# Optimization experiments

Measured on AMD Instinct MI355X. Metric: run time of the kernel, lower is better.

## Reference

```python
import jax, jax.numpy as jnp
import numpy as np

EMBED_DIM = 512
BLOCK = 511
N_HEAD = 8
N_GLOBAL = 4
N_LOCAL = 2
N_MIX = 2
RECEP = 4
T = 2 * BLOCK + 2  # [task, clip, BLOCK upper, BLOCK lower]
HD = EMBED_DIM // N_HEAD
NEG = -1e9


def _build_masks():
    bs = BLOCK
    temporal = np.concatenate([np.zeros(2), np.arange(bs) * 2 + 1, np.arange(bs) * 2 + 2])
    seq = temporal[None, :] <= temporal[:, None]  # causal over interleaved temporal order
    tq = np.concatenate([np.arange(bs) * 2 + 1 - 2 * RECEP + 1] * 2)
    tk = np.concatenate([np.arange(bs) * 2 + 1] * 2)
    de = tk[None, :] < tq[:, None]  # keys too far in the past for the sliding window
    local = seq.copy()
    local[2:, 2:] = local[2:, 2:] & ~de
    return jnp.asarray(local), jnp.asarray(seq)


LOCAL_MASK, GLOBAL_MASK = _build_masks()  # (T, T) bool, True = visible


def _linear_params(key, fan_in, fan_out):
    k1, k2 = jax.random.split(key)
    s = 1.0 / np.sqrt(fan_in)
    W = jax.random.uniform(k1, (fan_out, fan_in), minval=-s, maxval=s, dtype=jnp.float32)
    b = jax.random.uniform(k2, (fan_out,), minval=-s, maxval=s, dtype=jnp.float32)
    return W, b


def setup_inputs() -> dict:
    key = jax.random.key(0)
    ks = jax.random.split(key, 10)
    B = 4
    x = jax.random.normal(ks[0], (B, T, EMBED_DIM), dtype=jnp.float32)
    cond_mask = jnp.ones((B, T), dtype=jnp.float32)
    Wq, bq = _linear_params(ks[1], EMBED_DIM, EMBED_DIM)
    Wk, bk = _linear_params(ks[2], EMBED_DIM, EMBED_DIM)
    Wv, bv = _linear_params(ks[3], EMBED_DIM, EMBED_DIM)
    Wqml, bqml = _linear_params(ks[4], EMBED_DIM, HD * N_MIX)
    Wkml, bkml = _linear_params(ks[5], EMBED_DIM, HD * N_MIX)
    Wp, bp = _linear_params(ks[6], EMBED_DIM, EMBED_DIM)
    mix_w = jax.random.normal(ks[7], (N_MIX, 2), dtype=jnp.float32) * 0.5  # Conv2d(2*nm, nm, groups=nm, 1x1)
    bias_clip = jnp.full((1, N_HEAD, 1), 0.5, dtype=jnp.float32)
    bias_clip_ml = jnp.full((1, N_MIX, 1), 0.5, dtype=jnp.float32)
    return dict(x=x, cond_mask=cond_mask, Wq=Wq, bq=bq, Wk=Wk, bk=bk, Wv=Wv, bv=bv,
                Wqml=Wqml, bqml=bqml, Wkml=Wkml, bkml=bkml, mix_w=mix_w, Wp=Wp, bp=bp,
                bias_clip=bias_clip, bias_clip_ml=bias_clip_ml)


def reference(x, cond_mask, Wq, bq, Wk, bk, Wv, bv, Wqml, bqml, Wkml, bkml, mix_w, Wp, bp, bias_clip, bias_clip_ml):
    B, Tx, C = x.shape

    def heads(W, b, nh):
        return (x @ W.T + b).reshape(B, Tx, nh, HD).transpose(0, 2, 1, 3)  # (B, nh, T, hd)

    q = heads(Wq, bq, N_HEAD)
    k = heads(Wk, bk, N_HEAD)
    v = heads(Wv, bv, N_HEAD)
    qml = heads(Wqml, bqml, N_MIX)
    kml = heads(Wkml, bkml, N_MIX)

    scale = 1.0 / np.sqrt(HD)
    # main attention: heads [0:N_LOCAL] local-masked, rest global (causal) masked
    att = jnp.einsum('bhqd,bhkd->bhqk', q, k) * scale
    att = att.at[:, :, :, 1].add(bias_clip)  # learned bias on the CLIP-token key column
    head_mask = jnp.concatenate([
        jnp.broadcast_to(LOCAL_MASK, (N_LOCAL, Tx, Tx)),
        jnp.broadcast_to(GLOBAL_MASK, (N_MIX + N_GLOBAL, Tx, Tx))], axis=0)
    att = jax.nn.softmax(jnp.where(head_mask[None], att, NEG), axis=-1)

    # extra local-masked score maps for the mix heads
    aml = jnp.einsum('bhqd,bhkd->bhqk', qml, kml) * scale
    aml = aml.at[:, :, :, 1].add(bias_clip_ml)
    aml = jax.nn.softmax(jnp.where(LOCAL_MASK[None, None], aml, NEG), axis=-1)

    # grouped 1x1 conv: per mix head, blend (global, local) attention maps
    mix_in = jnp.stack([att[:, N_LOCAL:N_LOCAL + N_MIX], aml], axis=2)  # (B, nm, 2, T, T)
    mix_out = jnp.einsum('ho,bhoqk->bhqk', mix_w, mix_in)

    att_f = jnp.concatenate([att[:, :N_LOCAL], mix_out, att[:, N_LOCAL + N_MIX:]], axis=1)
    y = jnp.einsum('bhqk,bhkd->bhqd', att_f, v)
    y = y.transpose(0, 2, 1, 3).reshape(B, Tx, C)
    return y @ Wp.T + bp
```

## Files before the change

kernel.cpp:

```cpp
#include <hip/hip_runtime.h>

typedef unsigned short u16;
typedef __attribute__((ext_vector_type(8))) __bf16 bf16x8;
typedef __attribute__((ext_vector_type(4))) float f32x4;
typedef __attribute__((ext_vector_type(8))) short short8;
typedef __attribute__((ext_vector_type(4))) u16 us4;

#define T_SEQ 1024
#define PW 1280

__device__ __forceinline__ u16 f2bf(float f) {
  unsigned u = __float_as_uint(f);
  u += 0x7fff + ((u >> 16) & 1);
  return (u16)(u >> 16);
}
__device__ __forceinline__ float bf2f(u16 v) {
  return __uint_as_float((unsigned)v << 16);
}

__constant__ u16 GLOB_M[16] = {0x0101,0x0303,0x0707,0x0F0F,0x1F1F,0x3F3F,0x7F7F,0xFFFF,
                               0xFFFF,0x0307,0x070F,0x0F1F,0x1F3F,0x3F7F,0x7FFF,0xFFFF};
__constant__ u16 LOC_M[16]  = {0x0101,0x0303,0x0607,0x0C0D,0x1819,0x3031,0x6061,0xC0C1,
                               0x8183,0x0307,0x060F,0x0C1D,0x1839,0x3071,0x60E1,0xC1C1};

__device__ __forceinline__ void gll16(const u16* gp, u16* lp) {
  __builtin_amdgcn_global_load_lds((const __attribute__((address_space(1))) unsigned*)gp,
                                   (__attribute__((address_space(3))) unsigned*)lp, 16, 0, 0);
}

template<int NISS>
__device__ __forceinline__ void stage_sw(u16* lds, const u16* __restrict__ g,
                                         int ld, int tid) {
  const int w = tid >> 6;
#pragma unroll
  for (int i = 0; i < NISS; ++i) {
    int row = i * 32 + (tid >> 3);
    int cswz = ((tid & 7) << 4) ^ ((row & 7) << 4);
    gll16(g + (size_t)row * ld + (cswz >> 1), lds + i * 2048 + w * 512);
  }
}

__device__ __forceinline__ bf16x8 rd_sw(const u16* lds, int row, int colbyte) {
  return *(const bf16x8*)&lds[row * 64 + ((colbyte ^ ((row & 7) << 4)) >> 1)];
}

__global__ void prep_all(const float4* __restrict__ x, u16* __restrict__ xb,
                         const float* __restrict__ Wq, const float* __restrict__ Wk,
                         const float* __restrict__ Wv, const float* __restrict__ Wqml,
                         const float* __restrict__ Wkml, const float* __restrict__ Wp,
                         const float* __restrict__ bq, const float* __restrict__ bk,
                         const float* __restrict__ bv, const float* __restrict__ bqml,
                         const float* __restrict__ bkml,
                         u16* __restrict__ Wcat, u16* __restrict__ Wpx, float* __restrict__ bcat) {
  if (blockIdx.x < 2048) {
    int i = blockIdx.x * 256 + threadIdx.x;
    float4 v = x[i];
    us4 o = { f2bf(v.x), f2bf(v.y), f2bf(v.z), f2bf(v.w) };
    *(us4*)&xb[i * 4] = o;
    return;
  }
  int idx = (blockIdx.x - 2048) * 256 + threadIdx.x;
  const int NW = 1792 * 512;
  if (idx < NW) {
    int row = idx >> 9;
    float v;
    if (row < 512)       v = Wq[idx];
    else if (row < 1024) v = Wk[idx - 512 * 512];
    else if (row < 1536) v = Wv[idx - 1024 * 512];
    else if (row < 1664) v = Wqml[idx - 1536 * 512];
    else                 v = Wkml[idx - 1664 * 512];
    Wcat[idx] = f2bf(v);
    return;
  }
  int i2 = idx - NW;
  if (i2 < 512 * 640) {
    int n = i2 / 640, k2 = i2 - n * 640;
    float v = (k2 < 512) ? Wp[n * 512 + k2] : Wp[n * 512 + k2 - 384];
    Wpx[i2] = f2bf(v);
    return;
  }
  int i3 = i2 - 512 * 640;
  if (i3 < 1792) {
    float v;
    if (i3 < 512)       v = bq[i3];
    else if (i3 < 1024) v = bk[i3 - 512];
    else if (i3 < 1536) v = bv[i3 - 1024];
    else if (i3 < 1664) v = bqml[i3 - 1536];
    else                v = bkml[i3 - 1664];
    bcat[i3] = v;
  }
}

__global__ __launch_bounds__(256) void gemm_qkv(
    const u16* __restrict__ A, const u16* __restrict__ Bw,
    const float* __restrict__ bias, u16* __restrict__ Pout, u16* __restrict__ Vtb) {
  __shared__ u16 As[2][8192];
  __shared__ u16 Bs[2][8192];
  const int tid = threadIdx.x;
  const int lane = tid & 63, w = tid >> 6;
  const int g = lane >> 4, c = lane & 15;
  const int n0 = blockIdx.x * 128, m0 = blockIdx.y * 128;
  const int wm = (w >> 1) * 64, wn = (w & 1) * 64;

  f32x4 acc[4][4] = {};
  stage_sw<4>(As[0], A + (size_t)m0 * 512, 512, tid);
  stage_sw<4>(Bs[0], Bw + (size_t)n0 * 512, 512, tid);
  __syncthreads();
  for (int ks = 0; ks < 8; ++ks) {
    int cur = ks & 1;
    if (ks + 1 < 8) {
      stage_sw<4>(As[cur ^ 1], A + (size_t)m0 * 512 + (ks + 1) * 64, 512, tid);
      stage_sw<4>(Bs[cur ^ 1], Bw + (size_t)n0 * 512 + (ks + 1) * 64, 512, tid);
    }
#pragma unroll
    for (int h = 0; h < 2; ++h) {
      bf16x8 av[4], bv[4];
#pragma unroll
      for (int f = 0; f < 4; ++f) {
        av[f] = rd_sw(As[cur], wm + f * 16 + c, h * 64 + g * 16);
        bv[f] = rd_sw(Bs[cur], wn + f * 16 + c, h * 64 + g * 16);
      }
#pragma unroll
      for (int fm = 0; fm < 4; ++fm)
#pragma unroll
        for (int fn = 0; fn < 4; ++fn)
          acc[fm][fn] = __builtin_amdgcn_mfma_f32_16x16x32_bf16(av[fm], bv[fn], acc[fm][fn], 0, 0, 0);
    }
    __syncthreads();
  }

  const bool isV = (n0 >= 1024 && n0 < 1536);
#pragma unroll
  for (int fm = 0; fm < 4; ++fm)
#pragma unroll
    for (int fn = 0; fn < 4; ++fn) {
      int row = m0 + wm + fm * 16 + g * 4;
      int col = n0 + wn + fn * 16 + c;
      float bb = bias[col];
      if (isV) {
        int d = col - 1024;
        int bidx = row >> 10, t = row & 1023;
        us4 pack = { f2bf(acc[fm][fn][0] + bb), f2bf(acc[fm][fn][1] + bb),
                     f2bf(acc[fm][fn][2] + bb), f2bf(acc[fm][fn][3] + bb) };
        *(us4*)&Vtb[((size_t)bidx * 512 + d) * 1024 + t] = pack;
      } else {
        int pcol = (col < 1024) ? col : col - 512;
#pragma unroll
        for (int r = 0; r < 4; ++r)
          Pout[(size_t)(row + r) * PW + pcol] = f2bf(acc[fm][fn][r] + bb);
      }
    }
}

__global__ __launch_bounds__(256) void gemm_out(
    const u16* __restrict__ A, const u16* __restrict__ Bw,
    const float* __restrict__ bias, float* __restrict__ Cout) {
  __shared__ u16 As[2][8192];
  __shared__ u16 Bs[2][4096];
  const int tid = threadIdx.x;
  const int lane = tid & 63, w = tid >> 6;
  const int g = lane >> 4, c = lane & 15;
  const int n0 = blockIdx.x * 64, m0 = blockIdx.y * 128;
  const int wm = (w >> 1) * 64, wn = (w & 1) * 32;

  f32x4 acc[4][2] = {};
  stage_sw<4>(As[0], A + (size_t)m0 * 640, 640, tid);
  stage_sw<2>(Bs[0], Bw + (size_t)n0 * 640, 640, tid);
  __syncthreads();
  for (int ks = 0; ks < 10; ++ks) {
    int cur = ks & 1;
    if (ks + 1 < 10) {
      stage_sw<4>(As[cur ^ 1], A + (size_t)m0 * 640 + (ks + 1) * 64, 640, tid);
      stage_sw<2>(Bs[cur ^ 1], Bw + (size_t)n0 * 640 + (ks + 1) * 64, 640, tid);
    }
#pragma unroll
    for (int h = 0; h < 2; ++h) {
      bf16x8 av[4], bv[2];
#pragma unroll
      for (int f = 0; f < 4; ++f)
        av[f] = rd_sw(As[cur], wm + f * 16 + c, h * 64 + g * 16);
#pragma unroll
      for (int f = 0; f < 2; ++f)
        bv[f] = rd_sw(Bs[cur], wn + f * 16 + c, h * 64 + g * 16);
#pragma unroll
      for (int fm = 0; fm < 4; ++fm)
#pragma unroll
        for (int fn = 0; fn < 2; ++fn)
          acc[fm][fn] = __builtin_amdgcn_mfma_f32_16x16x32_bf16(av[fm], bv[fn], acc[fm][fn], 0, 0, 0);
    }
    __syncthreads();
  }
#pragma unroll
  for (int fm = 0; fm < 4; ++fm)
#pragma unroll
    for (int fn = 0; fn < 2; ++fn)
#pragma unroll
      for (int r = 0; r < 4; ++r) {
        int row = m0 + wm + fm * 16 + g * 4 + r;
        int col = n0 + wn + fn * 16 + c;
        Cout[(size_t)row * 512 + col] = acc[fm][fn][r] + bias[col];
      }
}

__global__ __launch_bounds__(256) void attn_k(
    const u16* __restrict__ P, const u16* __restrict__ Vtb, u16* __restrict__ Y,
    u16* __restrict__ Part_o, float* __restrict__ Part_ml,
    const float* __restrict__ mix_w, const float* __restrict__ bias_clip,
    const float* __restrict__ bias_clip_ml) {
  __shared__ u16 Ks[2][4096];
  __shared__ u16 Vs[2][4096];
  __shared__ u16 Ps[4][16][72];
  const int tid = threadIdx.x, lane = tid & 63, w = tid >> 6;
  const int g = lane >> 4, c = lane & 15;
  const int qt = blockIdx.x, u = blockIdx.y, b = blockIdx.z;

  int qcol, kcol, vsel, outcol = 0, slot = -1;
  bool localMask = false;
  float kbias, wgt = 1.0f;
  unsigned mask;
  if (u < 24) {
    int h = 2 + (u >> 2), sp = u & 3; slot = u;
    qcol = h * 64; kcol = 512 + h * 64; vsel = h; kbias = bias_clip[h];
    mask = (unsigned)GLOB_M[qt] & (0x1111u << sp);
  } else if (u < 26) {
    int h = u - 24;
    qcol = h * 64; kcol = 512 + h * 64; vsel = h; outcol = h * 64;
    localMask = true; kbias = bias_clip[h];
    mask = LOC_M[qt];
  } else {
    int mh = u - 26;
    qcol = 1024 + mh * 64; kcol = 1152 + mh * 64; vsel = 2 + mh; outcol = 512 + mh * 64;
    localMask = true; kbias = bias_clip_ml[mh]; wgt = mix_w[mh * 2 + 1];
    mask = LOC_M[qt];
  }
  const size_t baseP = (size_t)b * T_SEQ * PW;
  const u16* __restrict__ Kbase = P + baseP + kcol;
  const u16* __restrict__ Vbase = Vtb + ((size_t)b * 512 + vsel * 64) * 1024;
  const int r0 = qt * 64 + w * 16;

  int upmax[4], lomax[4], wminr[4];
#pragma unroll
  for (int r = 0; r < 4; ++r) {
    int row = r0 + g * 4 + r;
    int tqr = (row < 2) ? 0 : ((row < 513) ? 2 * row - 3 : 2 * row - 1024);
    upmax[r] = (tqr - 1) >> 1;
    lomax[r] = (tqr - 2) >> 1;
    wminr[r] = (localMask && row >= 2) ? ((row < 513 ? row - 2 : row - 513) - 3) : -1000000;
  }

  float m[4], l[4];
  f32x4 o[4] = {};
#pragma unroll
  for (int r = 0; r < 4; ++r) { m[r] = -1e8f; l[r] = 0.0f; }

  if (mask) {
    const int qrow = r0 + c;
    bf16x8 aq0 = *(const bf16x8*)&P[baseP + (size_t)qrow * PW + qcol + g * 8];
    bf16x8 aq1 = *(const bf16x8*)&P[baseP + (size_t)qrow * PW + qcol + 32 + g * 8];

    unsigned rem = mask;
    int kt = __ffs(rem) - 1; rem &= rem - 1;
    stage_sw<2>(Ks[0], Kbase + (size_t)(kt * 64) * PW, PW, tid);
    stage_sw<2>(Vs[0], Vbase + kt * 64, 1024, tid);
    __syncthreads();
    int cur = 0;

    for (;;) {
      int ktn = -1;
      if (rem) {
        ktn = __ffs(rem) - 1; rem &= rem - 1;
        stage_sw<2>(Ks[cur ^ 1], Kbase + (size_t)(ktn * 64) * PW, PW, tid);
        stage_sw<2>(Vs[cur ^ 1], Vbase + ktn * 64, 1024, tid);
      }

      const int k0 = kt * 64;
      float s[4][4];
#pragma unroll
      for (int cb = 0; cb < 4; ++cb) {
        f32x4 accs = {};
        bf16x8 bk0 = rd_sw(Ks[cur], cb * 16 + c, g * 16);
        bf16x8 bk1 = rd_sw(Ks[cur], cb * 16 + c, 64 + g * 16);
        accs = __builtin_amdgcn_mfma_f32_16x16x32_bf16(aq0, bk0, accs, 0, 0, 0);
        accs = __builtin_amdgcn_mfma_f32_16x16x32_bf16(aq1, bk1, accs, 0, 0, 0);
#pragma unroll
        for (int r = 0; r < 4; ++r) s[cb][r] = accs[r] * 0.125f;
      }
#pragma unroll
      for (int cb = 0; cb < 4; ++cb) {
        int colg = k0 + cb * 16 + c;
        bool tok = colg < 2;
        bool low = colg >= 513;
        int jk = colg - (low ? 513 : 2);
        float addb = (colg == 1) ? kbias : 0.0f;
#pragma unroll
        for (int r = 0; r < 4; ++r) {
          int bnd = low ? lomax[r] : upmax[r];
          bool vis = tok | ((jk <= bnd) & (jk >= wminr[r]));
          s[cb][r] = vis ? (s[cb][r] + addb) : -1e9f;
        }
      }
#pragma unroll
      for (int r = 0; r < 4; ++r) {
        float rmax = fmaxf(fmaxf(s[0][r], s[1][r]), fmaxf(s[2][r], s[3][r]));
        for (int off = 1; off < 16; off <<= 1)
          rmax = fmaxf(rmax, __shfl_xor(rmax, off));
        float mnew = fmaxf(m[r], rmax);
        float fr = __expf(m[r] - mnew);
        float psum = 0.0f;
#pragma unroll
        for (int cb = 0; cb < 4; ++cb) {
          float p = __expf(s[cb][r] - mnew);
          s[cb][r] = p;
          psum += p;
        }
        for (int off = 1; off < 16; off <<= 1)
          psum += __shfl_xor(psum, off);
        l[r] = l[r] * fr + psum;
        m[r] = mnew;
#pragma unroll
        for (int db = 0; db < 4; ++db) o[db][r] *= fr;
      }
#pragma unroll
      for (int cb = 0; cb < 4; ++cb)
#pragma unroll
        for (int r = 0; r < 4; ++r)
          Ps[w][g * 4 + r][cb * 16 + c] = f2bf(s[cb][r]);
      asm volatile("s_waitcnt lgkmcnt(0)" ::: "memory");
      __builtin_amdgcn_sched_barrier(0);
#pragma unroll
      for (int ks2 = 0; ks2 < 2; ++ks2) {
        bf16x8 ap = *(const bf16x8*)&Ps[w][c][ks2 * 32 + g * 8];
#pragma unroll
        for (int db = 0; db < 4; ++db) {
          bf16x8 bv = rd_sw(Vs[cur], db * 16 + c, ks2 * 64 + g * 16);
          o[db] = __builtin_amdgcn_mfma_f32_16x16x32_bf16(ap, bv, o[db], 0, 0, 0);
        }
      }

      if (ktn < 0) break;
      __syncthreads();
      cur ^= 1; kt = ktn;
    }
  }

  if (slot >= 0) {
    u16* po = Part_o + ((size_t)(slot * 4 + b)) * T_SEQ * 64;
#pragma unroll
    for (int r = 0; r < 4; ++r) {
      int row = r0 + g * 4 + r;
#pragma unroll
      for (int db = 0; db < 4; ++db)
        po[(size_t)row * 64 + db * 16 + c] = f2bf(o[db][r]);
      if (c == 0) {
        size_t mlb = (((size_t)(slot * 4 + b)) * T_SEQ + row) * 2;
        Part_ml[mlb] = m[r];
        Part_ml[mlb + 1] = l[r];
      }
    }
  } else {
    float wl[4];
#pragma unroll
    for (int r = 0; r < 4; ++r) wl[r] = wgt / l[r];
#pragma unroll
    for (int db = 0; db < 4; ++db)
#pragma unroll
      for (int r = 0; r < 4; ++r) {
        int row = r0 + g * 4 + r;
        int col = outcol + db * 16 + c;
        Y[((size_t)b * T_SEQ + row) * 640 + col] = f2bf(o[db][r] * wl[r]);
      }
  }
}

__global__ __launch_bounds__(256) void combine_k(
    const u16* __restrict__ Part_o, const float* __restrict__ Part_ml,
    u16* __restrict__ Y, const float* __restrict__ mix_w) {
  int idx = blockIdx.x * 256 + threadIdx.x;
  int q4 = idx & 15;
  int row = (idx >> 4) & 1023;
  int bb = (idx >> 14) & 3;
  int hp = idx >> 16;
  float mv[4], lv[4];
  float ms = -1e30f;
#pragma unroll
  for (int s = 0; s < 4; ++s) {
    size_t base = (((size_t)(hp * 4 + s) * 4 + bb) * 1024 + row) * 2;
    mv[s] = Part_ml[base];
    lv[s] = Part_ml[base + 1];
    ms = fmaxf(ms, mv[s]);
  }
  float denom = 0.0f, e[4];
#pragma unroll
  for (int s = 0; s < 4; ++s) { e[s] = __expf(mv[s] - ms); denom += lv[s] * e[s]; }
  float wgt = (hp < 2) ? mix_w[hp * 2] : 1.0f;
  float inv = wgt / denom;
  float out[4] = {0.f, 0.f, 0.f, 0.f};
#pragma unroll
  for (int s = 0; s < 4; ++s) {
    us4 ov = *(const us4*)&Part_o[(((size_t)(hp * 4 + s) * 4 + bb) * 1024 + row) * 64 + q4 * 4];
#pragma unroll
    for (int j = 0; j < 4; ++j) out[j] += e[s] * bf2f(ov[j]);
  }
  us4 pk = { f2bf(out[0] * inv), f2bf(out[1] * inv), f2bf(out[2] * inv), f2bf(out[3] * inv) };
  *(us4*)&Y[((size_t)bb * 1024 + row) * 640 + (hp + 2) * 64 + q4 * 4] = pk;
}

extern "C" void kernel_launch(void* const* d_in, const int* in_sizes, int n_in,
                              void* d_out, int out_size, void* d_ws, size_t ws_size,
                              hipStream_t stream) {
  const float* x     = (const float*)d_in[0];
  const float* Wq    = (const float*)d_in[2];
  const float* bq    = (const float*)d_in[3];
  const float* Wk    = (const float*)d_in[4];
  const float* bk    = (const float*)d_in[5];
  const float* Wv    = (const float*)d_in[6];
  const float* bv    = (const float*)d_in[7];
  const float* Wqml  = (const float*)d_in[8];
  const float* bqml  = (const float*)d_in[9];
  const float* Wkml  = (const float*)d_in[10];
  const float* bkml  = (const float*)d_in[11];
  const float* mixw  = (const float*)d_in[12];
  const float* Wp    = (const float*)d_in[13];
  const float* bp    = (const float*)d_in[14];
  const float* bclip = (const float*)d_in[15];
  const float* bclipml = (const float*)d_in[16];

  u16* xb   = (u16*)d_ws;
  u16* Wcat = xb + 4096 * 512;
  u16* Wpx  = Wcat + 1792 * 512;
  u16* Ybuf = Wpx + 512 * 640;
  u16* Vtb  = Ybuf + 4096 * 640;
  u16* Pbuf = Vtb + 4 * 512 * 1024;
  float* bcat = (float*)(Pbuf + 4096 * 1280);
  u16* Part_o = (u16*)(bcat + 2048);
  float* Part_ml = (float*)(Part_o + 24 * 4 * 1024 * 64);

  prep_all<<<6919, 256, 0, stream>>>((const float4*)x, xb, Wq, Wk, Wv, Wqml, Wkml, Wp,
                                     bq, bk, bv, bqml, bkml, Wcat, Wpx, bcat);
  gemm_qkv<<<dim3(14, 32), 256, 0, stream>>>(xb, Wcat, bcat, Pbuf, Vtb);
  attn_k<<<dim3(16, 28, 4), 256, 0, stream>>>(Pbuf, Vtb, Ybuf, Part_o, Part_ml,
                                              mixw, bclip, bclipml);
  combine_k<<<1536, 256, 0, stream>>>(Part_o, Part_ml, Ybuf, mixw);
  gemm_out<<<dim3(8, 32), 256, 0, stream>>>(Ybuf, Wpx, bp, (float*)d_out);
}
```

Baseline: 83.66 us.

## Transpose attention MFMA layout, load V into registers, drop double buffering

Swaps the MFMA operand order so the score and output tiles are transposed: each lane now owns one query row. The row max and sum reductions shrink from 16-lane shuffle trees to two cross-group shuffles, and the P and output stores become packed 4-element vector writes. V tiles are read straight from global memory into registers instead of being staged in shared memory. The K/V double buffer is replaced by a single K buffer with two barriers per tile, which cuts LDS use and may raise occupancy, but K loads no longer overlap with compute.

```diff
diff --git a/kernel.cpp b/kernel.cpp
--- a/kernel.cpp
+++ b/kernel.cpp
@@ -207,9 +207,8 @@
     u16* __restrict__ Part_o, float* __restrict__ Part_ml,
     const float* __restrict__ mix_w, const float* __restrict__ bias_clip,
     const float* __restrict__ bias_clip_ml) {
-  __shared__ u16 Ks[2][4096];
-  __shared__ u16 Vs[2][4096];
-  __shared__ u16 Ps[4][16][72];
+  __shared__ u16 Ks[4096];
+  __shared__ u16 Ps[4][16 * 72];
   const int tid = threadIdx.x, lane = tid & 63, w = tid >> 6;
   const int g = lane >> 4, c = lane & 15;
   const int qt = blockIdx.x, u = blockIdx.y, b = blockIdx.z;
@@ -237,138 +236,128 @@
   const u16* __restrict__ Kbase = P + baseP + kcol;
   const u16* __restrict__ Vbase = Vtb + ((size_t)b * 512 + vsel * 64) * 1024;
   const int r0 = qt * 64 + w * 16;
-
-  int upmax[4], lomax[4], wminr[4];
-#pragma unroll
-  for (int r = 0; r < 4; ++r) {
-    int row = r0 + g * 4 + r;
-    int tqr = (row < 2) ? 0 : ((row < 513) ? 2 * row - 3 : 2 * row - 1024);
-    upmax[r] = (tqr - 1) >> 1;
-    lomax[r] = (tqr - 2) >> 1;
-    wminr[r] = (localMask && row >= 2) ? ((row < 513 ? row - 2 : row - 513) - 3) : -1000000;
-  }
-
-  float m[4], l[4];
+  const int qg = r0 + c;
+
+  int tq = (qg < 2) ? 0 : ((qg < 513) ? 2 * qg - 3 : 2 * qg - 1024);
+  int upmax = (tq - 1) >> 1;
+  int lomax = (tq - 2) >> 1;
+  int wmin = (localMask && qg >= 2) ? ((qg < 513 ? qg - 2 : qg - 513) - 3) : -1000000;
+
+  float mM = -1e8f, lL = 0.0f;
   f32x4 o[4] = {};
-#pragma unroll
-  for (int r = 0; r < 4; ++r) { m[r] = -1e8f; l[r] = 0.0f; }
 
   if (mask) {
-    const int qrow = r0 + c;
-    bf16x8 aq0 = *(const bf16x8*)&P[baseP + (size_t)qrow * PW + qcol + g * 8];
-    bf16x8 aq1 = *(const bf16x8*)&P[baseP + (size_t)qrow * PW + qcol + 32 + g * 8];
+    bf16x8 aq0 = *(const bf16x8*)&P[baseP + (size_t)qg * PW + qcol + g * 8];
+    bf16x8 aq1 = *(const bf16x8*)&P[baseP + (size_t)qg * PW + qcol + 32 + g * 8];
 
     unsigned rem = mask;
     int kt = __ffs(rem) - 1; rem &= rem - 1;
-    stage_sw<2>(Ks[0], Kbase + (size_t)(kt * 64) * PW, PW, tid);
-    stage_sw<2>(Vs[0], Vbase + kt * 64, 1024, tid);
-    __syncthreads();
-    int cur = 0;
 
     for (;;) {
-      int ktn = -1;
-      if (rem) {
-        ktn = __ffs(rem) - 1; rem &= rem - 1;
-        stage_sw<2>(Ks[cur ^ 1], Kbase + (size_t)(ktn * 64) * PW, PW, tid);
-        stage_sw<2>(Vs[cur ^ 1], Vbase + ktn * 64, 1024, tid);
-      }
-
       const int k0 = kt * 64;
+      bf16x8 vr[2][4];
+#pragma unroll
+      for (int ks2 = 0; ks2 < 2; ++ks2)
+#pragma unroll
+        for (int db = 0; db < 4; ++db)
+          vr[ks2][db] = *(const bf16x8*)&Vbase[(size_t)(db * 16 + c) * 1024 + k0 + ks2 * 32 + g * 8];
+      stage_sw<2>(Ks, Kbase + (size_t)k0 * PW, PW, tid);
+      __syncthreads();
+
       float s[4][4];
 #pragma unroll
       for (int cb = 0; cb < 4; ++cb) {
         f32x4 accs = {};
-        bf16x8 bk0 = rd_sw(Ks[cur], cb * 16 + c, g * 16);
-        bf16x8 bk1 = rd_sw(Ks[cur], cb * 16 + c, 64 + g * 16);
-        accs = __builtin_amdgcn_mfma_f32_16x16x32_bf16(aq0, bk0, accs, 0, 0, 0);
-        accs = __builtin_amdgcn_mfma_f32_16x16x32_bf16(aq1, bk1, accs, 0, 0, 0);
+        bf16x8 bk0 = rd_sw(Ks, cb * 16 + c, g * 16);
+        bf16x8 bk1 = rd_sw(Ks, cb * 16 + c, 64 + g * 16);
+        accs = __builtin_amdgcn_mfma_f32_16x16x32_bf16(bk0, aq0, accs, 0, 0, 0);
+        accs = __builtin_amdgcn_mfma_f32_16x16x32_bf16(bk1, aq1, accs, 0, 0, 0);
 #pragma unroll
         for (int r = 0; r < 4; ++r) s[cb][r] = accs[r] * 0.125f;
       }
+      __syncthreads();
+
 #pragma unroll
       for (int cb = 0; cb < 4; ++cb) {
-        int colg = k0 + cb * 16 + c;
-        bool tok = colg < 2;
-        bool low = colg >= 513;
-        int jk = colg - (low ? 513 : 2);
-        float addb = (colg == 1) ? kbias : 0.0f;
+        int kb = k0 + cb * 16 + g * 4;
 #pragma unroll
         for (int r = 0; r < 4; ++r) {
-          int bnd = low ? lomax[r] : upmax[r];
-          bool vis = tok | ((jk <= bnd) & (jk >= wminr[r]));
+          int kk = kb + r;
+          bool tok = kk < 2;
+          bool low = kk >= 513;
+          int jk = kk - (low ? 513 : 2);
+          int bnd = low ? lomax : upmax;
+          bool vis = tok | ((jk <= bnd) & (jk >= wmin));
+          float addb = (kk == 1) ? kbias : 0.0f;
           s[cb][r] = vis ? (s[cb][r] + addb) : -1e9f;
         }
       }
-#pragma unroll
-      for (int r = 0; r < 4; ++r) {
-        float rmax = fmaxf(fmaxf(s[0][r], s[1][r]), fmaxf(s[2][r], s[3][r]));
-        for (int off = 1; off < 16; off <<= 1)
-          rmax = fmaxf(rmax, __shfl_xor(rmax, off));
-        float mnew = fmaxf(m[r], rmax);
-        float fr = __expf(m[r] - mnew);
-        float psum = 0.0f;
-#pragma unroll
-        for (int cb = 0; cb < 4; ++cb) {
+
+      float rmax = s[0][0];
+#pragma unroll
+      for (int cb = 0; cb < 4; ++cb)
+#pragma unroll
+        for (int r = 0; r < 4; ++r) rmax = fmaxf(rmax, s[cb][r]);
+      rmax = fmaxf(rmax, __shfl_xor(rmax, 16));
+      rmax = fmaxf(rmax, __shfl_xor(rmax, 32));
+      float mnew = fmaxf(mM, rmax);
+      float fr = __expf(mM - mnew);
+      float psum = 0.0f;
+#pragma unroll
+      for (int cb = 0; cb < 4; ++cb)
+#pragma unroll
+        for (int r = 0; r < 4; ++r) {
           float p = __expf(s[cb][r] - mnew);
           s[cb][r] = p;
           psum += p;
         }
-        for (int off = 1; off < 16; off <<= 1)
-          psum += __shfl_xor(psum, off);
-        l[r] = l[r] * fr + psum;
-        m[r] = mnew;
-#pragma unroll
-        for (int db = 0; db < 4; ++db) o[db][r] *= fr;
-      }
-#pragma unroll
-      for (int cb = 0; cb < 4; ++cb)
-#pragma unroll
-        for (int r = 0; r < 4; ++r)
-          Ps[w][g * 4 + r][cb * 16 + c] = f2bf(s[cb][r]);
+      psum += __shfl_xor(psum, 16);
+      psum += __shfl_xor(psum, 32);
+      lL = lL * fr + psum;
+      mM = mnew;
+#pragma unroll
+      for (int db = 0; db < 4; ++db) o[db] *= fr;
+
+#pragma unroll
+      for (int cb = 0; cb < 4; ++cb) {
+        us4 pk = { f2bf(s[cb][0]), f2bf(s[cb][1]), f2bf(s[cb][2]), f2bf(s[cb][3]) };
+        *(us4*)&Ps[w][c * 72 + cb * 16 + g * 4] = pk;
+      }
       asm volatile("s_waitcnt lgkmcnt(0)" ::: "memory");
       __builtin_amdgcn_sched_barrier(0);
+
 #pragma unroll
       for (int ks2 = 0; ks2 < 2; ++ks2) {
-        bf16x8 ap = *(const bf16x8*)&Ps[w][c][ks2 * 32 + g * 8];
-#pragma unroll
-        for (int db = 0; db < 4; ++db) {
-          bf16x8 bv = rd_sw(Vs[cur], db * 16 + c, ks2 * 64 + g * 16);
-          o[db] = __builtin_amdgcn_mfma_f32_16x16x32_bf16(ap, bv, o[db], 0, 0, 0);
-        }
-      }
-
-      if (ktn < 0) break;
-      __syncthreads();
-      cur ^= 1; kt = ktn;
+        bf16x8 ap = *(const bf16x8*)&Ps[w][c * 72 + ks2 * 32 + g * 8];
+#pragma unroll
+        for (int db = 0; db < 4; ++db)
+          o[db] = __builtin_amdgcn_mfma_f32_16x16x32_bf16(vr[ks2][db], ap, o[db], 0, 0, 0);
+      }
+
+      if (!rem) break;
+      kt = __ffs(rem) - 1; rem &= rem - 1;
     }
   }
 
   if (slot >= 0) {
     u16* po = Part_o + ((size_t)(slot * 4 + b)) * T_SEQ * 64;
 #pragma unroll
-    for (int r = 0; r < 4; ++r) {
-      int row = r0 + g * 4 + r;
-#pragma unroll
-      for (int db = 0; db < 4; ++db)
-        po[(size_t)row * 64 + db * 16 + c] = f2bf(o[db][r]);
-      if (c == 0) {
-        size_t mlb = (((size_t)(slot * 4 + b)) * T_SEQ + row) * 2;
-        Part_ml[mlb] = m[r];
-        Part_ml[mlb + 1] = l[r];
-      }
+    for (int db = 0; db < 4; ++db) {
+      us4 pk = { f2bf(o[db][0]), f2bf(o[db][1]), f2bf(o[db][2]), f2bf(o[db][3]) };
+      *(us4*)&po[(size_t)qg * 64 + db * 16 + g * 4] = pk;
+    }
+    if (g == 0) {
+      float2 ml = { mM, lL };
+      *(float2*)&Part_ml[(((size_t)(slot * 4 + b)) * T_SEQ + qg) * 2] = ml;
     }
   } else {
-    float wl[4];
-#pragma unroll
-    for (int r = 0; r < 4; ++r) wl[r] = wgt / l[r];
-#pragma unroll
-    for (int db = 0; db < 4; ++db)
-#pragma unroll
-      for (int r = 0; r < 4; ++r) {
-        int row = r0 + g * 4 + r;
-        int col = outcol + db * 16 + c;
-        Y[((size_t)b * T_SEQ + row) * 640 + col] = f2bf(o[db][r] * wl[r]);
-      }
+    float wl = wgt / lL;
+#pragma unroll
+    for (int db = 0; db < 4; ++db) {
+      us4 pk = { f2bf(o[db][0] * wl), f2bf(o[db][1] * wl),
+                 f2bf(o[db][2] * wl), f2bf(o[db][3] * wl) };
+      *(us4*)&Y[((size_t)b * T_SEQ + qg) * 640 + outcol + db * 16 + g * 4] = pk;
+    }
   }
 }
 
```

Result: slower. 88.68 us (+6.0%).
